# Optimization experiments

Measured on AMD Instinct MI355X. Metric: run time of the kernel, lower is better.

## Reference

```python
import jax, jax.numpy as jnp
import numpy as np

C_M = 256
C = 32
C_Z = 128
EPS = 1e-5


def setup_inputs() -> dict:
    key = jax.random.key(0)
    ks = jax.random.split(key, 8)
    b, s, i = 1, 128, 256
    msa = jax.random.normal(ks[0], (b, s, i, C_M), dtype=jnp.float32)
    scale_in = 1.0 / np.sqrt(C_M)
    scale_out = 1.0 / np.sqrt(C * C)
    return {
        "msa_representation": msa,
        "ln_w": jnp.ones((C_M,), jnp.float32),
        "ln_b": jnp.zeros((C_M,), jnp.float32),
        "w_left": jax.random.normal(ks[1], (C_M, C), jnp.float32) * scale_in,
        "b_left": jax.random.normal(ks[2], (C,), jnp.float32) * scale_in,
        "w_right": jax.random.normal(ks[3], (C_M, C), jnp.float32) * scale_in,
        "b_right": jax.random.normal(ks[4], (C,), jnp.float32) * scale_in,
        "w_out": jax.random.normal(ks[5], (C * C, C_Z), jnp.float32) * scale_out,
        "b_out": jax.random.normal(ks[6], (C_Z,), jnp.float32) * scale_out,
    }


def reference(msa_representation, ln_w, ln_b, w_left, b_left, w_right, b_right, w_out, b_out):
    x = msa_representation
    # LayerNorm over c_m
    mu = jnp.mean(x, axis=-1, keepdims=True)
    var = jnp.mean(jnp.square(x - mu), axis=-1, keepdims=True)
    x = (x - mu) * jax.lax.rsqrt(var + EPS) * ln_w + ln_b
    # dual projections: [b, s, i, c]
    A = x @ w_left + b_left
    B = x @ w_right + b_right
    s_dim = x.shape[1]
    # outer product mean over MSA depth s: [b, i, j, c, c]
    outer = jnp.einsum('bsic,bsjd->bijcd', A, B) / s_dim
    b_, i_, j_ = outer.shape[0], outer.shape[1], outer.shape[2]
    flat = outer.reshape(b_, i_, j_, C * C)
    return flat @ w_out + b_out
```

## Files before the change

kernel.cpp:

```cpp
#include <hip/hip_runtime.h>

typedef __attribute__((ext_vector_type(8))) short short8;
typedef __attribute__((ext_vector_type(4))) float f32x4;

#define CM 256
#define CC 32
#define CZ 128
#define SDIM 128
#define IDIM 256

__device__ __forceinline__ unsigned short f2bf(float f) {
  union { float f; unsigned u; } v; v.f = f;
  unsigned r = v.u + 0x7fffu + ((v.u >> 16) & 1u);
  return (unsigned short)(r >> 16);
}
__device__ __forceinline__ unsigned pack_bf2(float a, float b) {
  union { float f; unsigned u; } x, y; x.f = a; y.f = b;
  return ((x.u + 0x8000u) >> 16) | ((y.u + 0x8000u) & 0xffff0000u);
}

__global__ void k_prep(const float* __restrict__ wl, const float* __restrict__ wr,
                       const float* __restrict__ wo,
                       unsigned short* __restrict__ wlrT2, unsigned short* __restrict__ WF) {
  int t = blockIdx.x * 256 + threadIdx.x;
  if (t < 2048) {
    int frag = t >> 6, lane = t & 63;
    int nt = frag >> 3, ks = frag & 7;
    int ln = lane & 15, qd = lane >> 4;
    int c64 = nt * 16 + ln;
#pragma unroll
    for (int e = 0; e < 8; ++e) {
      int cm = ks * 32 + qd * 8 + e;
      float v = (c64 < CC) ? wl[cm * CC + c64] : wr[cm * CC + (c64 - CC)];
      wlrT2[(size_t)t * 8 + e] = f2bf(v);
    }
  } else {
    int t2 = t - 2048;
    if (t2 < 8 * 32 * 64) {
      int zt = t2 >> 11, ks = (t2 >> 6) & 31, lane = t2 & 63;
      int ln = lane & 15, qd = lane >> 4;
      int z = zt * 16 + ln;
#pragma unroll
      for (int e = 0; e < 8; ++e) {
        int c = qd * 8 + e, d = ks;
        WF[(size_t)t2 * 8 + e] = f2bf(wo[(c * 32 + d) * CZ + z] * (1.0f / 128.0f));
      }
    }
  }
}

__global__ __launch_bounds__(256) void k_lnproj(
    const float* __restrict__ x, const float* __restrict__ lnw, const float* __restrict__ lnb,
    const float* __restrict__ bl, const float* __restrict__ br,
    const unsigned short* __restrict__ wlrT2,
    unsigned short* __restrict__ A2, unsigned short* __restrict__ Bbuf) {
  __shared__ __align__(16) unsigned short xn[64][264];
  __shared__ __align__(16) unsigned short sT[64][72];
  int tid = threadIdx.x;
  int lane = tid & 63, ww = tid >> 6;
  int qd = lane >> 4, ln = lane & 15;
  int i = blockIdx.x, sh = blockIdx.y;

  for (int rr = 0; rr < 16; ++rr) {
    int sl = ww * 16 + rr;
    int s = sh * 64 + sl;
    float4 v = ((const float4*)(x + ((size_t)s * IDIM + i) * CM))[lane];
    float s1 = v.x + v.y + v.z + v.w;
    float s2 = v.x * v.x + v.y * v.y + v.z * v.z + v.w * v.w;
#pragma unroll
    for (int off = 32; off; off >>= 1) {
      s1 += __shfl_xor(s1, off);
      s2 += __shfl_xor(s2, off);
    }
    float mu = s1 * (1.0f / 256.0f);
    float var = s2 * (1.0f / 256.0f) - mu * mu;
    float rs = rsqrtf(var + 1e-5f);
    float4 w4 = ((const float4*)lnw)[lane];
    float4 b4 = ((const float4*)lnb)[lane];
    ushort4 h;
    h.x = f2bf((v.x - mu) * rs * w4.x + b4.x);
    h.y = f2bf((v.y - mu) * rs * w4.y + b4.y);
    h.z = f2bf((v.z - mu) * rs * w4.z + b4.z);
    h.w = f2bf((v.w - mu) * rs * w4.w + b4.w);
    *(ushort4*)&xn[sl][lane * 4] = h;
  }
  __syncthreads();

  f32x4 acc[4];
#pragma unroll
  for (int nt = 0; nt < 4; ++nt) acc[nt] = (f32x4){0.f, 0.f, 0.f, 0.f};
#pragma unroll
  for (int ks = 0; ks < 8; ++ks) {
    short8 af = *(const short8*)&xn[ww * 16 + ln][ks * 32 + qd * 8];
#pragma unroll
    for (int nt = 0; nt < 4; ++nt) {
      short8 bf = *(const short8*)(wlrT2 + ((size_t)((nt * 8 + ks) * 64 + lane)) * 8);
      acc[nt] = __builtin_amdgcn_mfma_f32_16x16x32_bf16(af, bf, acc[nt], 0, 0, 0);
    }
  }
#pragma unroll
  for (int nt = 0; nt < 4; ++nt) {
    int c64 = nt * 16 + ln;
    float bias = (c64 < CC) ? bl[c64] : br[c64 - CC];
    ushort4 h;
    h.x = f2bf(acc[nt][0] + bias);
    h.y = f2bf(acc[nt][1] + bias);
    h.z = f2bf(acc[nt][2] + bias);
    h.w = f2bf(acc[nt][3] + bias);
    *(ushort4*)&sT[c64][ww * 16 + qd * 4] = h;
  }
  __syncthreads();

  {
    int rtloc = ww >> 1, ksl = ww & 1;
    short8 v = *(const short8*)&sT[rtloc * 16 + ln][ksl * 32 + qd * 8];
    *(short8*)(A2 + ((size_t)(((2 * i + rtloc) * 4 + (sh * 2 + ksl)) * 64 + lane)) * 8) = v;
  }
  {
    int row = tid >> 3, ch = tid & 7;
    short8 v = *(const short8*)&sT[CC + row][ch * 8];
    *(short8*)(Bbuf + ((size_t)(i * CC + row)) * SDIM + sh * 64 + ch * 8) = v;
  }
}

__global__ __launch_bounds__(1024) void k_main(
    const unsigned short* __restrict__ A2, const unsigned short* __restrict__ Bbuf,
    const unsigned short* __restrict__ WF, const float* __restrict__ bout,
    float* __restrict__ out) {
  extern __shared__ __align__(16) char lds[];
  unsigned short* sB = (unsigned short*)lds;
  unsigned short* sP = (unsigned short*)lds;
  float* redR = (float*)lds;
  int tid = threadIdx.x;
  int lane = tid & 63, ww = tid >> 6;
  int qd = lane >> 4, ln = lane & 15;
  int i0 = blockIdx.x * 8, j0 = blockIdx.y * 8;

#pragma unroll
  for (int t = 0; t < 4; ++t) {
    int idx = tid + t * 1024;
    int r = idx >> 4, ch = idx & 15;
    short8 v = *(const short8*)(Bbuf + (size_t)(j0 * CC + r) * SDIM + ch * 8);
    *(short8*)&sB[r * 136 + ch * 8] = v;
  }
  __syncthreads();

  int wy = ww >> 2, wx = ww & 3;
  f32x4 acc1[4][4];
#pragma unroll
  for (int a = 0; a < 4; ++a)
#pragma unroll
    for (int b = 0; b < 4; ++b) acc1[a][b] = (f32x4){0.f, 0.f, 0.f, 0.f};
#pragma unroll
  for (int ks = 0; ks < 4; ++ks) {
    short8 af[4];
#pragma unroll
    for (int ti = 0; ti < 4; ++ti)
      af[ti] = *(const short8*)(A2 + ((size_t)((i0 * 2 + wy * 4 + ti) * 4 + ks) * 64 + lane) * 8);
#pragma unroll
    for (int tj = 0; tj < 4; ++tj) {
      short8 bf = *(const short8*)&sB[(wx * 64 + tj * 16 + ln) * 136 + ks * 32 + qd * 8];
#pragma unroll
      for (int ti = 0; ti < 4; ++ti)
        acc1[ti][tj] = __builtin_amdgcn_mfma_f32_16x16x32_bf16(af[ti], bf, acc1[ti][tj], 0, 0, 0);
    }
  }
  __syncthreads();

#pragma unroll
  for (int ti = 0; ti < 4; ++ti) {
    int iloc = wy * 2 + (ti >> 1);
    int cbase = 16 * (ti & 1) + qd * 4;
    int cb = cbase >> 3;
#pragma unroll
    for (int tj = 0; tj < 4; ++tj) {
      int jloc = wx * 2 + (tj >> 1);
      int d = 16 * (tj & 1) + ln;
      int p = iloc * 8 + jloc;
      uint2 u;
      u.x = pack_bf2(acc1[ti][tj][0], acc1[ti][tj][1]);
      u.y = pack_bf2(acc1[ti][tj][2], acc1[ti][tj][3]);
      *(uint2*)&sP[p * 1032 + d * 32 + ((((d >> 1) & 3) ^ cb) * 8) + (cbase & 7)] = u;
    }
  }
  __syncthreads();

  int ztp = ww & 3, kq = ww >> 2;
  f32x4 acc2[2][4];
#pragma unroll
  for (int a = 0; a < 2; ++a)
#pragma unroll
    for (int b = 0; b < 4; ++b) acc2[a][b] = (f32x4){0.f, 0.f, 0.f, 0.f};
#pragma unroll
  for (int cc = 0; cc < 8; ++cc) {
    int ks = kq * 8 + cc;
    short8 afr[4];
#pragma unroll
    for (int mt = 0; mt < 4; ++mt)
      afr[mt] = *(const short8*)&sP[(mt * 16 + ln) * 1032 + ks * 32 + ((((ks >> 1) & 3) ^ qd) * 8)];
#pragma unroll
    for (int h2 = 0; h2 < 2; ++h2) {
      int zt = ztp * 2 + h2;
      short8 bfr = *(const short8*)(WF + ((size_t)(zt * 32 + ks) * 64 + lane) * 8);
#pragma unroll
      for (int mt = 0; mt < 4; ++mt)
        acc2[h2][mt] = __builtin_amdgcn_mfma_f32_16x16x32_bf16(bfr, afr[mt], acc2[h2][mt], 0, 0, 0);
    }
  }

  __syncthreads();
  if (kq >= 2) {
    int s = (kq - 2) * 4 + ztp;
#pragma unroll
    for (int h2 = 0; h2 < 2; ++h2)
#pragma unroll
      for (int mt = 0; mt < 4; ++mt)
        *(f32x4*)&redR[(((s * 2 + h2) * 4 + mt) << 8) + lane * 4] = acc2[h2][mt];
  }
  __syncthreads();
  if (kq < 2) {
    int s = kq * 4 + ztp;
#pragma unroll
    for (int h2 = 0; h2 < 2; ++h2)
#pragma unroll
      for (int mt = 0; mt < 4; ++mt)
        acc2[h2][mt] += *(const f32x4*)&redR[(((s * 2 + h2) * 4 + mt) << 8) + lane * 4];
  }
  __syncthreads();
  if (kq == 1) {
    int s = ztp;
#pragma unroll
    for (int h2 = 0; h2 < 2; ++h2)
#pragma unroll
      for (int mt = 0; mt < 4; ++mt)
        *(f32x4*)&redR[(((s * 2 + h2) * 4 + mt) << 8) + lane * 4] = acc2[h2][mt];
  }
  __syncthreads();
  if (kq == 0) {
    int s = ztp;
#pragma unroll
    for (int h2 = 0; h2 < 2; ++h2) {
      int z = (ztp * 2 + h2) * 16 + qd * 4;
      f32x4 bz = *(const f32x4*)(bout + z);
#pragma unroll
      for (int mt = 0; mt < 4; ++mt) {
        int p = mt * 16 + ln;
        f32x4 v = acc2[h2][mt] +
                  *(const f32x4*)&redR[(((s * 2 + h2) * 4 + mt) << 8) + lane * 4] + bz;
        int i = i0 + (p >> 3), j = j0 + (p & 7);
        *(f32x4*)&out[((size_t)i * IDIM + j) * CZ + z] = v;
      }
    }
  }
}

extern "C" void kernel_launch(void* const* d_in, const int* in_sizes, int n_in,
                              void* d_out, int out_size, void* d_ws, size_t ws_size,
                              hipStream_t stream) {
  const float* msa = (const float*)d_in[0];
  const float* lnw = (const float*)d_in[1];
  const float* lnb = (const float*)d_in[2];
  const float* wl  = (const float*)d_in[3];
  const float* bl  = (const float*)d_in[4];
  const float* wr  = (const float*)d_in[5];
  const float* br  = (const float*)d_in[6];
  const float* wo  = (const float*)d_in[7];
  const float* bo  = (const float*)d_in[8];
  float* out = (float*)d_out;

  char* ws = (char*)d_ws;
  unsigned short* A2    = (unsigned short*)ws;
  unsigned short* Bbuf  = (unsigned short*)(ws + (2u << 20));
  unsigned short* wlrT2 = (unsigned short*)(ws + (4u << 20));
  unsigned short* WF    = (unsigned short*)(ws + (4u << 20) + 32768);

  (void)hipFuncSetAttribute((const void*)k_main,
                            hipFuncAttributeMaxDynamicSharedMemorySize, 132096);

  k_prep<<<72, 256, 0, stream>>>(wl, wr, wo, wlrT2, WF);
  k_lnproj<<<dim3(256, 2), 256, 0, stream>>>(msa, lnw, lnb, bl, br, wlrT2, A2, Bbuf);
  k_main<<<dim3(32, 32), 1024, 132096, stream>>>(A2, Bbuf, WF, bo, out);
}
```

Before: 141.6 us.

## Halve k_main tile to 8x4 pairs with 512 threads for more resident blocks

k_main now covers 8 i by 4 j per block instead of 8x8, using 512 threads and half the dynamic LDS (about 66 KB instead of 132 KB), with twice as many blocks in the grid. The second GEMM's wave work split changes from 2 z-tiles x 4 m-tiles to 4 z-tiles x 2 m-tiles, and the reduction indexing is rewritten to match. The aim is to fit several blocks per CU (launch_bounds 512,4) so LDS use and latency hiding improve. In exchange, each block reuses A2 fragments and WF loads across fewer outputs, so global and L2 traffic for those operands roughly doubles.

```diff
diff --git a/kernel.cpp b/kernel.cpp
--- a/kernel.cpp
+++ b/kernel.cpp
@@ -123,29 +123,29 @@
   }
 }
 
-__global__ __launch_bounds__(1024) void k_main(
+__global__ __launch_bounds__(512, 4) void k_main(
     const unsigned short* __restrict__ A2, const unsigned short* __restrict__ Bbuf,
     const unsigned short* __restrict__ WF, const float* __restrict__ bout,
     float* __restrict__ out) {
   extern __shared__ __align__(16) char lds[];
   unsigned short* sB = (unsigned short*)lds;
   unsigned short* sP = (unsigned short*)lds;
-  float* redR = (float*)lds;
+  float* redF = (float*)lds;
   int tid = threadIdx.x;
   int lane = tid & 63, ww = tid >> 6;
   int qd = lane >> 4, ln = lane & 15;
-  int i0 = blockIdx.x * 8, j0 = blockIdx.y * 8;
+  int i0 = blockIdx.x * 8, j0 = blockIdx.y * 4;
 
 #pragma unroll
   for (int t = 0; t < 4; ++t) {
-    int idx = tid + t * 1024;
+    int idx = tid + t * 512;
     int r = idx >> 4, ch = idx & 15;
     short8 v = *(const short8*)(Bbuf + (size_t)(j0 * CC + r) * SDIM + ch * 8);
     *(short8*)&sB[r * 136 + ch * 8] = v;
   }
   __syncthreads();
 
-  int wy = ww >> 2, wx = ww & 3;
+  int wy = ww >> 1, wx = ww & 1;
   f32x4 acc1[4][4];
 #pragma unroll
   for (int a = 0; a < 4; ++a)
@@ -176,7 +176,7 @@
     for (int tj = 0; tj < 4; ++tj) {
       int jloc = wx * 2 + (tj >> 1);
       int d = 16 * (tj & 1) + ln;
-      int p = iloc * 8 + jloc;
+      int p = iloc * 4 + jloc;
       uint2 u;
       u.x = pack_bf2(acc1[ti][tj][0], acc1[ti][tj][1]);
       u.y = pack_bf2(acc1[ti][tj][2], acc1[ti][tj][3]);
@@ -185,69 +185,67 @@
   }
   __syncthreads();
 
-  int ztp = ww & 3, kq = ww >> 2;
-  f32x4 acc2[2][4];
-#pragma unroll
-  for (int a = 0; a < 2; ++a)
-#pragma unroll
-    for (int b = 0; b < 4; ++b) acc2[a][b] = (f32x4){0.f, 0.f, 0.f, 0.f};
+  int ztg = ww >> 2, kq = ww & 3;
+  f32x4 acc2[4][2];
+#pragma unroll
+  for (int a = 0; a < 4; ++a)
+#pragma unroll
+    for (int b = 0; b < 2; ++b) acc2[a][b] = (f32x4){0.f, 0.f, 0.f, 0.f};
 #pragma unroll
   for (int cc = 0; cc < 8; ++cc) {
     int ks = kq * 8 + cc;
-    short8 afr[4];
-#pragma unroll
-    for (int mt = 0; mt < 4; ++mt)
+    short8 afr[2];
+#pragma unroll
+    for (int mt = 0; mt < 2; ++mt)
       afr[mt] = *(const short8*)&sP[(mt * 16 + ln) * 1032 + ks * 32 + ((((ks >> 1) & 3) ^ qd) * 8)];
 #pragma unroll
-    for (int h2 = 0; h2 < 2; ++h2) {
-      int zt = ztp * 2 + h2;
+    for (int z4 = 0; z4 < 4; ++z4) {
+      int zt = ztg * 4 + z4;
       short8 bfr = *(const short8*)(WF + ((size_t)(zt * 32 + ks) * 64 + lane) * 8);
 #pragma unroll
-      for (int mt = 0; mt < 4; ++mt)
-        acc2[h2][mt] = __builtin_amdgcn_mfma_f32_16x16x32_bf16(bfr, afr[mt], acc2[h2][mt], 0, 0, 0);
+      for (int mt = 0; mt < 2; ++mt)
+        acc2[z4][mt] = __builtin_amdgcn_mfma_f32_16x16x32_bf16(bfr, afr[mt], acc2[z4][mt], 0, 0, 0);
     }
   }
 
   __syncthreads();
   if (kq >= 2) {
-    int s = (kq - 2) * 4 + ztp;
-#pragma unroll
-    for (int h2 = 0; h2 < 2; ++h2)
-#pragma unroll
-      for (int mt = 0; mt < 4; ++mt)
-        *(f32x4*)&redR[(((s * 2 + h2) * 4 + mt) << 8) + lane * 4] = acc2[h2][mt];
+    int s = (kq - 2) * 2 + ztg;
+#pragma unroll
+    for (int z4 = 0; z4 < 4; ++z4)
+#pragma unroll
+      for (int mt = 0; mt < 2; ++mt)
+        *(f32x4*)&redF[s * 2048 + ((z4 * 2 + mt) << 8) + lane * 4] = acc2[z4][mt];
   }
   __syncthreads();
   if (kq < 2) {
-    int s = kq * 4 + ztp;
-#pragma unroll
-    for (int h2 = 0; h2 < 2; ++h2)
-#pragma unroll
-      for (int mt = 0; mt < 4; ++mt)
-        acc2[h2][mt] += *(const f32x4*)&redR[(((s * 2 + h2) * 4 + mt) << 8) + lane * 4];
+    int s = kq * 2 + ztg;
+#pragma unroll
+    for (int z4 = 0; z4 < 4; ++z4)
+#pragma unroll
+      for (int mt = 0; mt < 2; ++mt)
+        acc2[z4][mt] += *(const f32x4*)&redF[s * 2048 + ((z4 * 2 + mt) << 8) + lane * 4];
   }
   __syncthreads();
   if (kq == 1) {
-    int s = ztp;
-#pragma unroll
-    for (int h2 = 0; h2 < 2; ++h2)
-#pragma unroll
-      for (int mt = 0; mt < 4; ++mt)
-        *(f32x4*)&redR[(((s * 2 + h2) * 4 + mt) << 8) + lane * 4] = acc2[h2][mt];
+#pragma unroll
+    for (int z4 = 0; z4 < 4; ++z4)
+#pragma unroll
+      for (int mt = 0; mt < 2; ++mt)
+        *(f32x4*)&redF[ztg * 2048 + ((z4 * 2 + mt) << 8) + lane * 4] = acc2[z4][mt];
   }
   __syncthreads();
   if (kq == 0) {
-    int s = ztp;
-#pragma unroll
-    for (int h2 = 0; h2 < 2; ++h2) {
-      int z = (ztp * 2 + h2) * 16 + qd * 4;
+#pragma unroll
+    for (int z4 = 0; z4 < 4; ++z4) {
+      int z = (ztg * 4 + z4) * 16 + qd * 4;
       f32x4 bz = *(const f32x4*)(bout + z);
 #pragma unroll
-      for (int mt = 0; mt < 4; ++mt) {
+      for (int mt = 0; mt < 2; ++mt) {
         int p = mt * 16 + ln;
-        f32x4 v = acc2[h2][mt] +
-                  *(const f32x4*)&redR[(((s * 2 + h2) * 4 + mt) << 8) + lane * 4] + bz;
-        int i = i0 + (p >> 3), j = j0 + (p & 7);
+        f32x4 v = acc2[z4][mt] +
+                  *(const f32x4*)&redF[ztg * 2048 + ((z4 * 2 + mt) << 8) + lane * 4] + bz;
+        int i = i0 + (p >> 2), j = j0 + (p & 3);
         *(f32x4*)&out[((size_t)i * IDIM + j) * CZ + z] = v;
       }
     }
@@ -275,9 +273,9 @@
   unsigned short* WF    = (unsigned short*)(ws + (4u << 20) + 32768);
 
   (void)hipFuncSetAttribute((const void*)k_main,
-                            hipFuncAttributeMaxDynamicSharedMemorySize, 132096);
+                            hipFuncAttributeMaxDynamicSharedMemorySize, 66048);
 
   k_prep<<<72, 256, 0, stream>>>(wl, wr, wo, wlrT2, WF);
   k_lnproj<<<dim3(256, 2), 256, 0, stream>>>(msa, lnw, lnb, bl, br, wlrT2, A2, Bbuf);
-  k_main<<<dim3(32, 32), 1024, 132096, stream>>>(A2, Bbuf, WF, bo, out);
-}
+  k_main<<<dim3(32, 64), 512, 66048, stream>>>(A2, Bbuf, WF, bo, out);
+}
```

Measured after the change: 143.9 us. Within noise of the previous version (+1.6%).
